# Performance work log

Measured on AMD Instinct MI355X. Metric: run time of the kernel, lower is better.

The kernel has to match this reference:

```python
import jax, jax.numpy as jnp
import numpy as np

RADIUS = 4
SIGMA_X = 5.0
SIGMA_I = 1.0


def gaussian_kernel3d():
    # norm.pdf(d)/norm.pdf(0) == exp(-d^2/2)
    r = RADIUS
    n = 2 * r + 1
    v = np.linspace(-r, r, n) ** 2
    xy, yz, zx = np.meshgrid(v, v, v)
    dist = (xy + yz + zx) / SIGMA_X
    k = np.exp(-0.5 * dist ** 2).astype(np.float32)  # (9,9,9)
    return jnp.asarray(k)


def setup_inputs() -> dict:
    key = jax.random.key(0)
    k1, k2 = jax.random.split(key)
    B, C, K, D, H, W = 2, 1, 5, 96, 96, 96
    inputs = jax.random.normal(k1, (B, C, D, H, W), jnp.float32)
    logits = jax.random.normal(k2, (B, K, D, H, W), jnp.float32)
    labels = jax.nn.softmax(logits, axis=1)  # class probabilities
    return {"inputs": inputs, "labels": labels}


def reference(inputs, labels):
    # inputs: [B,C,D,H,W] raw image; labels: [B,K,D,H,W] class probs
    K = labels.shape[1]
    kernel = gaussian_kernel3d()
    eps_m, eps_d = 1e-5, 1e-6

    # per-class, per-channel weighted mean: [B,K,C]
    num_mean = jnp.mean(inputs[:, None] * labels[:, :, None], axis=(3, 4, 5))
    den_mean = jnp.mean(labels, axis=(2, 3, 4))[..., None] + eps_m  # [B,K,1]
    class_mean = num_mean / den_mean  # [B,K,C]

    # diff: sum over channels of (x - mean)^2 -> [B,K,D,H,W]
    diff = jnp.sum((inputs[:, None] - class_mean[..., None, None, None]) ** 2, axis=2)
    weights = jnp.exp(-(diff ** 2) / (SIGMA_I ** 2))  # [B,K,D,H,W]

    # depthwise (per-class) 3D conv with the shared Gaussian kernel
    rhs = jnp.broadcast_to(kernel[None, None], (K, 1) + kernel.shape)  # [K,1,9,9,9]
    pad = [(RADIUS, RADIUS)] * 3

    def conv(x):  # x: [B,K,D,H,W]
        return jax.lax.conv_general_dilated(
            x, rhs, window_strides=(1, 1, 1), padding=pad,
            dimension_numbers=("NCDHW", "OIDHW", "NCDHW"),
            feature_group_count=K)

    numer = jnp.sum(labels * conv(labels * weights), axis=(0, 2, 3, 4))  # [K]
    denom = jnp.sum(labels * conv(weights), axis=(0, 2, 3, 4))  # [K]
    loss = jnp.sum(jnp.abs(numer / (denom + eps_d)))  # L1Loss vs zeros per class
    return jnp.asarray(K, inputs.dtype) - loss
```

## Files before the change

kernel.cpp:

```cpp
#include <hip/hip_runtime.h>
#include <math.h>

#define VOL (96*96*96)
#define KCLS 5
#define CZ 12
#define PSTR 64
#define PROWS 40
#define PSZ (PROWS*PSTR)
#define NS2 15

typedef __attribute__((ext_vector_type(8))) short bf16x8;
typedef __attribute__((ext_vector_type(4))) float f32x4;
typedef __attribute__((ext_vector_type(4))) unsigned short us4;

constexpr int S2VALS[NS2] = {0,1,2,4,5,8,9,10,13,16,17,18,20,25,32};
constexpr int MAP33[33] = {0,1,2,-1,3,4,-1,-1,5,6,7,-1,-1,8,-1,-1,
                           9,10,11,-1,12,-1,-1,-1,-1,13,-1,-1,-1,-1,-1,-1,14};

__device__ __forceinline__ unsigned short f2bf(float f) {
  unsigned u = __builtin_bit_cast(unsigned, f);
  u += 0x7fffu + ((u >> 16) & 1u);
  return (unsigned short)(u >> 16);
}


__global__ __launch_bounds__(256) void k_sums(const float* __restrict__ I,
                                              const float* __restrict__ L,
                                              double* __restrict__ ws) {
  const int b = blockIdx.y;
  const int base = blockIdx.x * 2048 + threadIdx.x;
  const float4* __restrict__ I4 = (const float4*)(I + b * VOL);
  float4 iv[8];
#pragma unroll
  for (int j = 0; j < 8; ++j) iv[j] = I4[base + j * 256];
  float sL[KCLS], sIL[KCLS];
#pragma unroll
  for (int k = 0; k < KCLS; ++k) { sL[k] = 0.f; sIL[k] = 0.f; }
#pragma unroll 1
  for (int k = 0; k < KCLS; ++k) {
    const float4* __restrict__ L4 = (const float4*)(L + (b * KCLS + k) * VOL);
#pragma unroll
    for (int j = 0; j < 8; ++j) {
      float4 lv = L4[base + j * 256];
      sL[k] += (lv.x + lv.y) + (lv.z + lv.w);
      sIL[k] += iv[j].x * lv.x + iv[j].y * lv.y + iv[j].z * lv.z + iv[j].w * lv.w;
    }
  }
#pragma unroll
  for (int k = 0; k < KCLS; ++k) {
#pragma unroll
    for (int off = 32; off; off >>= 1) {
      sL[k] += __shfl_down(sL[k], off);
      sIL[k] += __shfl_down(sIL[k], off);
    }
  }
  __shared__ double red[4][2 * KCLS];
  const int wid = threadIdx.x >> 6;
  if ((threadIdx.x & 63) == 0) {
#pragma unroll
    for (int k = 0; k < KCLS; ++k) {
      red[wid][k] = (double)sL[k];
      red[wid][KCLS + k] = (double)sIL[k];
    }
  }
  __syncthreads();
  if (threadIdx.x < 2 * KCLS) {
    double v = red[0][threadIdx.x] + red[1][threadIdx.x] + red[2][threadIdx.x] + red[3][threadIdx.x];
    const int k = threadIdx.x % KCLS;
    const int which = threadIdx.x / KCLS;
    atomicAdd(&ws[(which ? 10 : 0) + b * KCLS + k], v);
  }
}

__global__ __launch_bounds__(256, 2) void k_conv(const float* __restrict__ I,
                                                 const float* __restrict__ L,
                                                 double* __restrict__ ws) {
  __shared__ __attribute__((aligned(16))) short AtabF[NS2 * 64 * 8];
  __shared__ __attribute__((aligned(16))) short Wp[2][PSZ];
  __shared__ __attribute__((aligned(16))) short LWp[2][PSZ];
  __shared__ double red[8];

  const int t = threadIdx.x;
  const int vol = blockIdx.z;
  const int kcl = vol % KCLS;
  const int b = vol / KCLS;
  const int x0 = (blockIdx.x % 3) * 32;
  const int y0 = (blockIdx.x / 3) * 32;
  const int z0 = blockIdx.y * CZ;

  const float* __restrict__ Ib = I + b * VOL;
  const float* __restrict__ Lb = L + vol * VOL;

  const double sLd = ws[vol];
  const float mean = (float)(ws[10 + vol] / (sLd + 1e-5 * (double)VOL));

#pragma unroll
  for (int s2i = 0; s2i < NS2; ++s2i) {
    const float s2c = (float)S2VALS[s2i];
#pragma unroll
    for (int h = 0; h < 2; ++h) {
      const int sub = t + h * 256;
      const int lane_ = sub >> 3;
      const int j = sub & 7;
      const int dx = ((lane_ >> 4) << 3) + j - (lane_ & 15);
      float val = 0.f;
      if (dx >= 0 && dx <= 8) {
        const float q = s2c + (float)((dx - 4) * (dx - 4));
        val = __expf(-0.02f * q * q);
      }
      AtabF[s2i * 512 + sub] = (short)f2bf(val);
    }
  }

  const int lane = t & 63;
  const int w = t >> 6;
  const int wx = w & 1, wy = w >> 1;
  const int nn = lane & 15, qq = lane >> 4;

  f32x4 accW[9], accL[9];
  const f32x4 zer = {0.f, 0.f, 0.f, 0.f};
#pragma unroll
  for (int i = 0; i < 9; ++i) { accW[i] = zer; accL[i] = zer; }
  float pN = 0.f, pD = 0.f;

  auto loadQuad = [&](int zp, int qi, float4& iv, float4& lv, bool& ok) {
    const int row = qi / 12;
    const int xq = (qi - row * 12) * 4;
    const int gy = y0 - 4 + row, gx = x0 - 4 + xq;
    ok = ((unsigned)zp < 96u) && ((unsigned)gy < 96u) && ((unsigned)gx <= 92u);
    if (ok) {
      const int off = (zp * 96 + gy) * 96 + gx;
      iv = *(const float4*)(Ib + off);
      lv = *(const float4*)(Lb + off);
    } else {
      iv = make_float4(0.f, 0.f, 0.f, 0.f);
      lv = make_float4(0.f, 0.f, 0.f, 0.f);
    }
  };
  auto storeQuad = [&](int buf, int qi, const float4& iv, const float4& lv, bool ok) {
    const int row = qi / 12;
    const int q = qi - row * 12;
    const int c = q >> 1, o = (q & 1) << 2;
    const int a = row * PSTR + (((c ^ (row & 7)) << 3) + o);
    float d, w0, w1, w2, w3;
    d = iv.x - mean; d = d * d; w0 = ok ? __expf(-d * d) : 0.f;
    d = iv.y - mean; d = d * d; w1 = ok ? __expf(-d * d) : 0.f;
    d = iv.z - mean; d = d * d; w2 = ok ? __expf(-d * d) : 0.f;
    d = iv.w - mean; d = d * d; w3 = ok ? __expf(-d * d) : 0.f;
    us4 wv = { f2bf(w0), f2bf(w1), f2bf(w2), f2bf(w3) };
    us4 ov = { f2bf(lv.x * w0), f2bf(lv.y * w1), f2bf(lv.z * w2), f2bf(lv.w * w3) };
    *(us4*)(&Wp[buf][a]) = wv;
    *(us4*)(&LWp[buf][a]) = ov;
  };

  {
    float4 i0, l0, i1, l1; bool o0, o1;
    loadQuad(z0 - 4, t, i0, l0, o0);
    storeQuad(0, t, i0, l0, o0);
    if (t < 224) { loadQuad(z0 - 4, 256 + t, i1, l1, o1); storeQuad(0, 256 + t, i1, l1, o1); }
  }
  __syncthreads();

  bf16x8 afr[NS2];
#pragma unroll
  for (int r = 0; r < NS2; ++r)
    afr[r] = *(const bf16x8*)(AtabF + (r * 64 + lane) * 8);

  auto computeFull = [&](int buf) {
    const short* __restrict__ Wb = Wp[buf];
    const short* __restrict__ Lwb = LWp[buf];
#pragma unroll
    for (int dy = 0; dy < 9; ++dy) {
      const int dy2c = (dy - 4) * (dy - 4);
      const int yrow = 16 * wy + nn + dy;
      const int boff = yrow * PSTR + ((((2 * wx + qq) ^ (yrow & 7))) << 3);
      const bf16x8 bw = *(const bf16x8*)(Wb + boff);
      const bf16x8 bl = *(const bf16x8*)(Lwb + boff);
#pragma unroll
      for (int i = 0; i < 9; ++i) {
        const int da = (i < 4) ? (4 - i) : (i - 4);
        const int ri = MAP33[dy2c + da * da];
        accW[i] = __builtin_amdgcn_mfma_f32_16x16x32_bf16(afr[ri], bw, accW[i], 0, 0, 0);
        accL[i] = __builtin_amdgcn_mfma_f32_16x16x32_bf16(afr[ri], bl, accL[i], 0, 0, 0);
      }
    }
  };
  auto computeEdge = [&](int buf, int iLo, int iHi) {
    const short* __restrict__ Wb = Wp[buf];
    const short* __restrict__ Lwb = LWp[buf];
#pragma unroll
    for (int dy = 0; dy < 9; ++dy) {
      const int dy2c = (dy - 4) * (dy - 4);
      const int yrow = 16 * wy + nn + dy;
      const int boff = yrow * PSTR + ((((2 * wx + qq) ^ (yrow & 7))) << 3);
      const bf16x8 bw = *(const bf16x8*)(Wb + boff);
      const bf16x8 bl = *(const bf16x8*)(Lwb + boff);
#pragma unroll
      for (int i = 0; i < 9; ++i) {
        if (i >= iLo && i <= iHi) {
          const int da = (i < 4) ? (4 - i) : (i - 4);
          const int ri = MAP33[dy2c + da * da];
          accW[i] = __builtin_amdgcn_mfma_f32_16x16x32_bf16(afr[ri], bw, accW[i], 0, 0, 0);
          accL[i] = __builtin_amdgcn_mfma_f32_16x16x32_bf16(afr[ri], bl, accL[i], 0, 0, 0);
        }
      }
    }
  };

  auto retire = [&](int zo) {
    if (zo >= z0 && zo < z0 + CZ) {
      const int gy = y0 + 16 * wy + nn;
      const int gx = x0 + 16 * wx + 4 * qq;
      const float4 lab = *(const float4*)(Lb + (zo * 96 + gy) * 96 + gx);
      pN += accL[0].x * lab.x + accL[0].y * lab.y + accL[0].z * lab.z + accL[0].w * lab.w;
      pD += accW[0].x * lab.x + accW[0].y * lab.y + accW[0].z * lab.z + accW[0].w * lab.w;
    }
#pragma unroll
    for (int i = 0; i < 8; ++i) { accW[i] = accW[i + 1]; accL[i] = accL[i + 1]; }
    accW[8] = zer; accL[8] = zer;
  };

  const int zp0 = z0 - 4;
  const int zend = z0 + CZ + 4;
  for (int zp = zp0; zp < zend; ++zp) {
    const int cur = (zp - zp0) & 1;
    const bool more = (zp + 1 < zend);
    float4 i0, l0, i1, l1; bool o0 = false, o1 = false;
    if (more) {
      loadQuad(zp + 1, t, i0, l0, o0);
      if (t < 224) loadQuad(zp + 1, 256 + t, i1, l1, o1);
    }
    int iLo = z0 - (zp - 4); if (iLo < 0) iLo = 0;
    int iHi = (z0 + CZ - 1) - (zp - 4); if (iHi > 8) iHi = 8;
    if (iLo == 0 && iHi == 8) computeFull(cur);
    else computeEdge(cur, iLo, iHi);
    retire(zp - 4);
    if (more) {
      storeQuad(cur ^ 1, t, i0, l0, o0);
      if (t < 224) storeQuad(cur ^ 1, 256 + t, i1, l1, o1);
    }
    __syncthreads();
  }

#pragma unroll
  for (int off = 32; off; off >>= 1) {
    pN += __shfl_down(pN, off);
    pD += __shfl_down(pD, off);
  }
  if (lane == 0) { red[w] = (double)pN; red[4 + w] = (double)pD; }
  __syncthreads();
  if (t == 0) {
    atomicAdd(&ws[20 + kcl], red[0] + red[1] + red[2] + red[3]);
    atomicAdd(&ws[25 + kcl], red[4] + red[5] + red[6] + red[7]);
  }
}

__global__ void k_final(const double* __restrict__ ws, float* __restrict__ out) {
  if (threadIdx.x == 0 && blockIdx.x == 0) {
    double loss = 0.0;
    for (int k = 0; k < KCLS; ++k) {
      loss += fabs(ws[20 + k] / (ws[25 + k] + 1e-6));
    }
    out[0] = (float)(5.0 - loss);
  }
}

extern "C" void kernel_launch(void* const* d_in, const int* in_sizes, int n_in,
                              void* d_out, int out_size, void* d_ws, size_t ws_size,
                              hipStream_t stream) {
  (void)in_sizes; (void)n_in; (void)out_size; (void)ws_size;
  const float* I = (const float*)d_in[0];
  const float* L = (const float*)d_in[1];
  double* ws = (double*)d_ws;
  float* out = (float*)d_out;

  hipMemsetAsync(d_ws, 0, 32 * sizeof(double), stream);
  k_sums<<<dim3(108, 2, 1), 256, 0, stream>>>(I, L, ws);
  k_conv<<<dim3(9, 8, 10), 256, 0, stream>>>(I, L, ws);
  k_final<<<1, 64, 0, stream>>>(ws, out);
}
```

Baseline: 192.1 us.

## Shrink z-chunks, spread atomics over slots, compute filter fragments in registers

The z-chunk per block shrinks from 12 to 8 slices, raising the conv grid to 1080 blocks, and launch bounds request 4 blocks per CU. The shared filter table is removed and each lane builds its bf16 filter fragments directly in registers. The reduction kernel now launches one block per 256 float4s, and the global double atomics are spread across 32 or 16 slots per class, with the final kernel summing the slots. The boundary handling uses a single bounds-checked compute path and loads the label early. Smaller chunks mean a larger share of redundant 4-slice halo work per output, and higher occupancy may add register pressure.

Measured after the change: 454.4 us. 2.37x slower.

```diff
diff --git a/kernel.cpp b/kernel.cpp
--- a/kernel.cpp
+++ b/kernel.cpp
@@ -3,7 +3,7 @@
 
 #define VOL (96*96*96)
 #define KCLS 5
-#define CZ 12
+#define CZ 8
 #define PSTR 64
 #define PROWS 40
 #define PSZ (PROWS*PSTR)
@@ -28,23 +28,14 @@
                                               const float* __restrict__ L,
                                               double* __restrict__ ws) {
   const int b = blockIdx.y;
-  const int base = blockIdx.x * 2048 + threadIdx.x;
-  const float4* __restrict__ I4 = (const float4*)(I + b * VOL);
-  float4 iv[8];
-#pragma unroll
-  for (int j = 0; j < 8; ++j) iv[j] = I4[base + j * 256];
+  const int base = blockIdx.x * 256 + threadIdx.x;
+  const float4 iv = ((const float4*)(I + b * VOL))[base];
   float sL[KCLS], sIL[KCLS];
 #pragma unroll
-  for (int k = 0; k < KCLS; ++k) { sL[k] = 0.f; sIL[k] = 0.f; }
-#pragma unroll 1
   for (int k = 0; k < KCLS; ++k) {
-    const float4* __restrict__ L4 = (const float4*)(L + (b * KCLS + k) * VOL);
-#pragma unroll
-    for (int j = 0; j < 8; ++j) {
-      float4 lv = L4[base + j * 256];
-      sL[k] += (lv.x + lv.y) + (lv.z + lv.w);
-      sIL[k] += iv[j].x * lv.x + iv[j].y * lv.y + iv[j].z * lv.z + iv[j].w * lv.w;
-    }
+    const float4 lv = ((const float4*)(L + (b * KCLS + k) * VOL))[base];
+    sL[k] = (lv.x + lv.y) + (lv.z + lv.w);
+    sIL[k] = iv.x * lv.x + iv.y * lv.y + iv.z * lv.z + iv.w * lv.w;
   }
 #pragma unroll
   for (int k = 0; k < KCLS; ++k) {
@@ -68,17 +59,18 @@
     double v = red[0][threadIdx.x] + red[1][threadIdx.x] + red[2][threadIdx.x] + red[3][threadIdx.x];
     const int k = threadIdx.x % KCLS;
     const int which = threadIdx.x / KCLS;
-    atomicAdd(&ws[(which ? 10 : 0) + b * KCLS + k], v);
-  }
-}
-
-__global__ __launch_bounds__(256, 2) void k_conv(const float* __restrict__ I,
+    const int slot = blockIdx.x & 31;
+    atomicAdd(&ws[32 + which * 320 + (b * KCLS + k) * 32 + slot], v);
+  }
+}
+
+__global__ __launch_bounds__(256, 4) void k_conv(const float* __restrict__ I,
                                                  const float* __restrict__ L,
                                                  double* __restrict__ ws) {
-  __shared__ __attribute__((aligned(16))) short AtabF[NS2 * 64 * 8];
   __shared__ __attribute__((aligned(16))) short Wp[2][PSZ];
   __shared__ __attribute__((aligned(16))) short LWp[2][PSZ];
   __shared__ double red[8];
+  __shared__ float meanS;
 
   const int t = threadIdx.x;
   const int vol = blockIdx.z;
@@ -91,31 +83,43 @@
   const float* __restrict__ Ib = I + b * VOL;
   const float* __restrict__ Lb = L + vol * VOL;
 
-  const double sLd = ws[vol];
-  const float mean = (float)(ws[10 + vol] / (sLd + 1e-5 * (double)VOL));
-
-#pragma unroll
-  for (int s2i = 0; s2i < NS2; ++s2i) {
-    const float s2c = (float)S2VALS[s2i];
-#pragma unroll
-    for (int h = 0; h < 2; ++h) {
-      const int sub = t + h * 256;
-      const int lane_ = sub >> 3;
-      const int j = sub & 7;
-      const int dx = ((lane_ >> 4) << 3) + j - (lane_ & 15);
+  if (t < 64) {
+    double a = (t < 32) ? ws[32 + vol * 32 + t] : 0.0;
+    double c = (t < 32) ? ws[352 + vol * 32 + t] : 0.0;
+#pragma unroll
+    for (int off = 16; off; off >>= 1) {
+      a += __shfl_down(a, off);
+      c += __shfl_down(c, off);
+    }
+    if (t == 0) meanS = (float)(c / (a + 1e-5 * (double)VOL));
+  }
+  __syncthreads();
+  const float mean = meanS;
+
+  const int lane = t & 63;
+  const int w = t >> 6;
+  const int wx = w & 1, wy = w >> 1;
+  const int nn = lane & 15, qq = lane >> 4;
+  const int gyOut = y0 + 16 * wy + nn;
+  const int gxOut = x0 + 16 * wx + 4 * qq;
+
+  bf16x8 afr[NS2];
+#pragma unroll
+  for (int r = 0; r < NS2; ++r) {
+    const float s2c = (float)S2VALS[r];
+    bf16x8 v;
+#pragma unroll
+    for (int j = 0; j < 8; ++j) {
+      const int dx = 8 * qq + j - nn;
       float val = 0.f;
       if (dx >= 0 && dx <= 8) {
         const float q = s2c + (float)((dx - 4) * (dx - 4));
         val = __expf(-0.02f * q * q);
       }
-      AtabF[s2i * 512 + sub] = (short)f2bf(val);
-    }
-  }
-
-  const int lane = t & 63;
-  const int w = t >> 6;
-  const int wx = w & 1, wy = w >> 1;
-  const int nn = lane & 15, qq = lane >> 4;
+      v[j] = (short)f2bf(val);
+    }
+    afr[r] = v;
+  }
 
   f32x4 accW[9], accL[9];
   const f32x4 zer = {0.f, 0.f, 0.f, 0.f};
@@ -153,38 +157,6 @@
     *(us4*)(&LWp[buf][a]) = ov;
   };
 
-  {
-    float4 i0, l0, i1, l1; bool o0, o1;
-    loadQuad(z0 - 4, t, i0, l0, o0);
-    storeQuad(0, t, i0, l0, o0);
-    if (t < 224) { loadQuad(z0 - 4, 256 + t, i1, l1, o1); storeQuad(0, 256 + t, i1, l1, o1); }
-  }
-  __syncthreads();
-
-  bf16x8 afr[NS2];
-#pragma unroll
-  for (int r = 0; r < NS2; ++r)
-    afr[r] = *(const bf16x8*)(AtabF + (r * 64 + lane) * 8);
-
-  auto computeFull = [&](int buf) {
-    const short* __restrict__ Wb = Wp[buf];
-    const short* __restrict__ Lwb = LWp[buf];
-#pragma unroll
-    for (int dy = 0; dy < 9; ++dy) {
-      const int dy2c = (dy - 4) * (dy - 4);
-      const int yrow = 16 * wy + nn + dy;
-      const int boff = yrow * PSTR + ((((2 * wx + qq) ^ (yrow & 7))) << 3);
-      const bf16x8 bw = *(const bf16x8*)(Wb + boff);
-      const bf16x8 bl = *(const bf16x8*)(Lwb + boff);
-#pragma unroll
-      for (int i = 0; i < 9; ++i) {
-        const int da = (i < 4) ? (4 - i) : (i - 4);
-        const int ri = MAP33[dy2c + da * da];
-        accW[i] = __builtin_amdgcn_mfma_f32_16x16x32_bf16(afr[ri], bw, accW[i], 0, 0, 0);
-        accL[i] = __builtin_amdgcn_mfma_f32_16x16x32_bf16(afr[ri], bl, accL[i], 0, 0, 0);
-      }
-    }
-  };
   auto computeEdge = [&](int buf, int iLo, int iHi) {
     const short* __restrict__ Wb = Wp[buf];
     const short* __restrict__ Lwb = LWp[buf];
@@ -207,18 +179,13 @@
     }
   };
 
-  auto retire = [&](int zo) {
-    if (zo >= z0 && zo < z0 + CZ) {
-      const int gy = y0 + 16 * wy + nn;
-      const int gx = x0 + 16 * wx + 4 * qq;
-      const float4 lab = *(const float4*)(Lb + (zo * 96 + gy) * 96 + gx);
-      pN += accL[0].x * lab.x + accL[0].y * lab.y + accL[0].z * lab.z + accL[0].w * lab.w;
-      pD += accW[0].x * lab.x + accW[0].y * lab.y + accW[0].z * lab.z + accW[0].w * lab.w;
-    }
-#pragma unroll
-    for (int i = 0; i < 8; ++i) { accW[i] = accW[i + 1]; accL[i] = accL[i + 1]; }
-    accW[8] = zer; accL[8] = zer;
-  };
+  {
+    float4 i0, l0, i1, l1; bool o0, o1;
+    loadQuad(z0 - 4, t, i0, l0, o0);
+    storeQuad(0, t, i0, l0, o0);
+    if (t < 224) { loadQuad(z0 - 4, 256 + t, i1, l1, o1); storeQuad(0, 256 + t, i1, l1, o1); }
+  }
+  __syncthreads();
 
   const int zp0 = z0 - 4;
   const int zend = z0 + CZ + 4;
@@ -230,11 +197,24 @@
       loadQuad(zp + 1, t, i0, l0, o0);
       if (t < 224) loadQuad(zp + 1, 256 + t, i1, l1, o1);
     }
-    int iLo = z0 - (zp - 4); if (iLo < 0) iLo = 0;
-    int iHi = (z0 + CZ - 1) - (zp - 4); if (iHi > 8) iHi = 8;
-    if (iLo == 0 && iHi == 8) computeFull(cur);
-    else computeEdge(cur, iLo, iHi);
-    retire(zp - 4);
+    const int zo = zp - 4;
+    const bool lok = (zo >= z0) && (zo < z0 + CZ);
+    float4 lab = make_float4(0.f, 0.f, 0.f, 0.f);
+    if (lok) lab = *(const float4*)(Lb + (zo * 96 + gyOut) * 96 + gxOut);
+
+    if ((unsigned)zp <= 95u) {
+      int iLo = z0 - zo; if (iLo < 0) iLo = 0;
+      int iHi = (z0 + CZ - 1) - zo; if (iHi > 8) iHi = 8;
+      computeEdge(cur, iLo, iHi);
+    }
+    if (lok) {
+      pN += accL[0].x * lab.x + accL[0].y * lab.y + accL[0].z * lab.z + accL[0].w * lab.w;
+      pD += accW[0].x * lab.x + accW[0].y * lab.y + accW[0].z * lab.z + accW[0].w * lab.w;
+    }
+#pragma unroll
+    for (int i = 0; i < 8; ++i) { accW[i] = accW[i + 1]; accL[i] = accL[i + 1]; }
+    accW[8] = zer; accL[8] = zer;
+
     if (more) {
       storeQuad(cur ^ 1, t, i0, l0, o0);
       if (t < 224) storeQuad(cur ^ 1, 256 + t, i1, l1, o1);
@@ -250,17 +230,27 @@
   if (lane == 0) { red[w] = (double)pN; red[4 + w] = (double)pD; }
   __syncthreads();
   if (t == 0) {
-    atomicAdd(&ws[20 + kcl], red[0] + red[1] + red[2] + red[3]);
-    atomicAdd(&ws[25 + kcl], red[4] + red[5] + red[6] + red[7]);
+    const int slot = (blockIdx.x + blockIdx.y) & 15;
+    atomicAdd(&ws[672 + kcl * 16 + slot], red[0] + red[1] + red[2] + red[3]);
+    atomicAdd(&ws[752 + kcl * 16 + slot], red[4] + red[5] + red[6] + red[7]);
   }
 }
 
 __global__ void k_final(const double* __restrict__ ws, float* __restrict__ out) {
-  if (threadIdx.x == 0 && blockIdx.x == 0) {
-    double loss = 0.0;
-    for (int k = 0; k < KCLS; ++k) {
-      loss += fabs(ws[20 + k] / (ws[25 + k] + 1e-6));
-    }
+  __shared__ double acc[KCLS];
+  const int t = threadIdx.x;
+  if (t < KCLS) {
+    double n = 0.0, d = 0.0;
+#pragma unroll
+    for (int s = 0; s < 16; ++s) {
+      n += ws[672 + t * 16 + s];
+      d += ws[752 + t * 16 + s];
+    }
+    acc[t] = fabs(n / (d + 1e-6));
+  }
+  __syncthreads();
+  if (t == 0) {
+    double loss = acc[0] + acc[1] + acc[2] + acc[3] + acc[4];
     out[0] = (float)(5.0 - loss);
   }
 }
@@ -274,8 +264,8 @@
   double* ws = (double*)d_ws;
   float* out = (float*)d_out;
 
-  hipMemsetAsync(d_ws, 0, 32 * sizeof(double), stream);
-  k_sums<<<dim3(108, 2, 1), 256, 0, stream>>>(I, L, ws);
-  k_conv<<<dim3(9, 8, 10), 256, 0, stream>>>(I, L, ws);
+  hipMemsetAsync(d_ws, 0, 832 * sizeof(double), stream);
+  k_sums<<<dim3(864, 2, 1), 256, 0, stream>>>(I, L, ws);
+  k_conv<<<dim3(9, 12, 10), 256, 0, stream>>>(I, L, ws);
   k_final<<<1, 64, 0, stream>>>(ws, out);
 }
```
